# Optimization experiments

Measured on AMD Instinct MI355X. Metric: run time of the kernel, lower is better.

The kernel has to match this reference:

```python
import jax, jax.numpy as jnp
import numpy as np

B, T, V, E, H = 256, 512, 30000, 256, 32


def _run_dir(x, mask, Wih, Whh, bih, bhh, reverse):
    # x: [B,T,D], mask: [B,T] bool. PyTorch GRU gate order: r, z, n.
    gi = jnp.einsum('btd,gd->btg', x, Wih) + bih  # precompute input gates [B,T,3H]
    h0 = jnp.zeros((x.shape[0], Whh.shape[1]), x.dtype)

    def step(h, inp):
        gi_t, m_t = inp
        gh = h @ Whh.T + bhh
        ir, iz, inn = jnp.split(gi_t, 3, axis=-1)
        hr, hz, hn = jnp.split(gh, 3, axis=-1)
        r = jax.nn.sigmoid(ir + hr)
        z = jax.nn.sigmoid(iz + hz)
        n = jnp.tanh(inn + r * hn)
        h_new = (1.0 - z) * n + z * h
        # packed-sequence semantics: freeze state at padded steps
        h = jnp.where(m_t[:, None], h_new, h)
        return h, h

    hT, ys = jax.lax.scan(step, h0, (jnp.swapaxes(gi, 0, 1), mask.T), reverse=reverse)
    return jnp.swapaxes(ys, 0, 1), hT  # outputs [B,T,H], final hidden [B,H]


def _bigru_layer(x, mask, pf, pb):
    of, hf = _run_dir(x, mask, *pf, reverse=False)
    ob, hb = _run_dir(x, mask, *pb, reverse=True)
    return jnp.concatenate([of, ob], axis=-1), hf, hb


def setup_inputs() -> dict:
    key = jax.random.key(0)
    ks = jax.random.split(key, 24)
    lengths = jax.random.randint(ks[0], (B,), 1, T + 1)
    mask = (jnp.arange(T)[None, :] < lengths[:, None]).astype(jnp.int32)
    ids = jax.random.randint(ks[1], (B, T), 1, V)
    ids = jnp.where(mask > 0, ids, 0)  # pad_id = 0 at padded positions
    embed = (jax.random.normal(ks[2], (V, E), jnp.float32) * 0.1).at[0].set(0.0)

    def gru_params(k, din):
        k1, k2, k3, k4 = jax.random.split(k, 4)
        s = 1.0 / np.sqrt(H)
        return (jax.random.uniform(k1, (3 * H, din), jnp.float32, -s, s),
                jax.random.uniform(k2, (3 * H, H), jnp.float32, -s, s),
                jax.random.uniform(k3, (3 * H,), jnp.float32, -s, s),
                jax.random.uniform(k4, (3 * H,), jnp.float32, -s, s))

    inp = {"input_ids": ids, "attention_mask": mask, "embed": embed}
    i = 3
    for layer, din in (("l0", E), ("l1", 2 * H)):
        for d in ("f", "b"):
            Wih, Whh, bih, bhh = gru_params(ks[i], din); i += 1
            inp[f"Wih_{layer}{d}"] = Wih
            inp[f"Whh_{layer}{d}"] = Whh
            inp[f"bih_{layer}{d}"] = bih
            inp[f"bhh_{layer}{d}"] = bhh
    s = 1.0 / np.sqrt(2 * H)
    inp["Wout"] = jax.random.uniform(ks[i], (6, 2 * H), jnp.float32, -s, s)
    inp["bout"] = jax.random.uniform(ks[i + 1], (6,), jnp.float32, -s, s)
    return inp


def reference(input_ids, attention_mask, embed,
              Wih_l0f, Whh_l0f, bih_l0f, bhh_l0f,
              Wih_l0b, Whh_l0b, bih_l0b, bhh_l0b,
              Wih_l1f, Whh_l1f, bih_l1f, bhh_l1f,
              Wih_l1b, Whh_l1b, bih_l1b, bhh_l1b,
              Wout, bout):
    mask = attention_mask > 0
    x = embed[input_ids]  # [B,T,E]
    x1, _, _ = _bigru_layer(x, mask,
                            (Wih_l0f, Whh_l0f, bih_l0f, bhh_l0f),
                            (Wih_l0b, Whh_l0b, bih_l0b, bhh_l0b))
    # no dropout: eval-mode forward
    _, hf, hb = _bigru_layer(x1, mask,
                             (Wih_l1f, Whh_l1f, bih_l1f, bhh_l1f),
                             (Wih_l1b, Whh_l1b, bih_l1b, bhh_l1b))
    top = jnp.concatenate([hf, hb], axis=-1)  # h_n[-2:] -> [B, 2H]
    return top @ Wout.T + bout  # [B, 6]
```

## Files before the change

### kernel.cpp

```cpp
#include <hip/hip_runtime.h>
#include <hip/hip_bf16.h>
#include <stdint.h>

#define B_ 256
#define T_ 512
#define V_ 30000
#define E_ 256
#define H_ 32

typedef float v2f __attribute__((ext_vector_type(2)));

__device__ __forceinline__ float sigmoidf_fast(float x) {
    return 1.0f / (1.0f + __expf(-x));
}
__device__ __forceinline__ float tanhf_fast(float x) {
    return 1.0f - 2.0f / (1.0f + __expf(2.0f * x));
}
__device__ __forceinline__ uint32_t rlu(float v, int lane) {
    return (uint32_t)__builtin_amdgcn_readlane(__float_as_int(v), lane);
}
__device__ __forceinline__ void pk_fma(v2f& acc, v2f w, uint64_t hh) {
    asm("v_pk_fma_f32 %0, %1, %2, %0" : "+v"(acc) : "v"(w), "s"(hh));
}

#define GEMM_MT 64
#define GEMM_KC 32
#define GEMM_PA 68
#define GEMM_PB 196

__global__ __launch_bounds__(256) void gemm_gates(
    const float* __restrict__ A, int M, int K,
    const float* __restrict__ Wf, const float* __restrict__ Wb,
    const float* __restrict__ bihf, const float* __restrict__ bhhf,
    const float* __restrict__ bihb, const float* __restrict__ bhhb,
    float* __restrict__ Out)
{
    __shared__ float As[GEMM_KC][GEMM_PA];
    __shared__ float Bs[GEMM_KC][GEMM_PB];

    const int tid = threadIdx.x;
    const int mbase = blockIdx.x * GEMM_MT;
    const int mg = tid >> 5, ng = tid & 31;
    const int m_off = mg * 8, n_off = ng * 6;

    float acc[8][6];
    #pragma unroll
    for (int r = 0; r < 8; ++r)
        #pragma unroll
        for (int c = 0; c < 6; ++c) acc[r][c] = 0.f;

    for (int kc = 0; kc < K; kc += GEMM_KC) {
        #pragma unroll
        for (int i = 0; i < 2; ++i) {
            int fi = tid + 256 * i;
            int row = fi >> 3, cf = fi & 7;
            int m = mbase + row;
            float4 v = make_float4(0.f, 0.f, 0.f, 0.f);
            if (m < M) v = *(const float4*)&A[(size_t)m * K + kc + cf * 4];
            As[cf * 4 + 0][row] = v.x; As[cf * 4 + 1][row] = v.y;
            As[cf * 4 + 2][row] = v.z; As[cf * 4 + 3][row] = v.w;
        }
        #pragma unroll
        for (int i = 0; i < 6; ++i) {
            int fi = tid + 256 * i;
            int g = fi >> 3, cf = fi & 7;
            const float* Wsel = (g < 96) ? (Wf + (size_t)g * K)
                                         : (Wb + (size_t)(g - 96) * K);
            float4 v = *(const float4*)&Wsel[kc + cf * 4];
            Bs[cf * 4 + 0][g] = v.x; Bs[cf * 4 + 1][g] = v.y;
            Bs[cf * 4 + 2][g] = v.z; Bs[cf * 4 + 3][g] = v.w;
        }
        __syncthreads();
        #pragma unroll
        for (int k = 0; k < GEMM_KC; ++k) {
            float a[8], bb[6];
            *(float4*)&a[0] = *(const float4*)&As[k][m_off];
            *(float4*)&a[4] = *(const float4*)&As[k][m_off + 4];
            *(float2*)&bb[0] = *(const float2*)&Bs[k][n_off];
            *(float2*)&bb[2] = *(const float2*)&Bs[k][n_off + 2];
            *(float2*)&bb[4] = *(const float2*)&Bs[k][n_off + 4];
            #pragma unroll
            for (int r = 0; r < 8; ++r)
                #pragma unroll
                for (int c = 0; c < 6; ++c)
                    acc[r][c] = fmaf(a[r], bb[c], acc[r][c]);
        }
        __syncthreads();
    }

    float bias[6];
    #pragma unroll
    for (int c = 0; c < 6; ++c) {
        int g = n_off + c;
        int g96 = (g < 96) ? g : g - 96;
        const float* bih = (g < 96) ? bihf : bihb;
        const float* bhh = (g < 96) ? bhhf : bhhb;
        bias[c] = bih[g96] + ((g96 < 64) ? bhh[g96] : 0.f);
    }
    #pragma unroll
    for (int r = 0; r < 8; ++r) {
        int m = mbase + m_off + r;
        if (m < M) {
            float* op = &Out[(size_t)m * 192 + n_off];
            #pragma unroll
            for (int c = 0; c < 6; ++c) op[c] = acc[r][c] + bias[c];
        }
    }
}

template <int USE_IDS>
__global__ __launch_bounds__(64, 1) void gru_scan(
    const float* __restrict__ gi,
    const int* __restrict__ ids,
    const int* __restrict__ mask,
    const float* __restrict__ Whh_f, const float* __restrict__ Whh_b,
    const float* __restrict__ bhh_f, const float* __restrict__ bhh_b,
    float* __restrict__ out_seq,
    float* __restrict__ out_fin)
{
    const int l = threadIdx.x;
    const int j = l & 31;
    const bool lower = l < 32;
    const int dir = blockIdx.x & 1;
    const int b = blockIdx.x >> 1;
    const int bT = b * T_;

    const float* Whh = dir ? Whh_b : Whh_f;
    const float* bhh = dir ? bhh_b : bhh_f;

    v2f wR[16], wZ[16], wN[16];
    #pragma unroll
    for (int q = 0; q < 16; ++q) {
        wR[q] = *(const v2f*)&Whh[j * 32 + 2 * q];
        wZ[q] = *(const v2f*)&Whh[(32 + j) * 32 + 2 * q];
        wN[q] = *(const v2f*)&Whh[(64 + j) * 32 + 2 * q];
    }
    const float bn = bhh[64 + j];

    const int offR = dir * 96 + j;
    const int offZ = dir * 96 + 32 + j;
    const int offN = dir * 96 + 64 + j;

    auto wbase = [&](int c) { return dir ? (bT + 508 - 4 * c) : (bT + 4 * c); };

    int4 ids0 = make_int4(0, 0, 0, 0);
    if (USE_IDS) ids0 = *(const int4*)&ids[wbase(0)];
    int4 mask_use = *(const int4*)&mask[wbase(0)];
    int4 mask_mid = *(const int4*)&mask[wbase(1)];
    int4 mask_in  = make_int4(0, 0, 0, 0);
    int4 ids_pf = make_int4(0, 0, 0, 0), ids_mid = ids_pf, ids_in = ids_pf;
    if (USE_IDS) {
        ids_pf  = *(const int4*)&ids[wbase(1)];
        ids_mid = *(const int4*)&ids[wbase(2)];
    }

    float gR[2][4], gZ[2][4], gN[2][4];
    #pragma unroll
    for (int u = 0; u < 4; ++u) {
        int row;
        if (USE_IDS) {
            const int* ip = (const int*)&ids0;
            row = dir ? ip[3 - u] : ip[u];
        } else {
            row = bT + (dir ? (511 - u) : u);
        }
        const float* gp = gi + (size_t)row * 192;
        gR[0][u] = gp[offR];
        gZ[0][u] = gp[offZ];
        gN[0][u] = gp[offN];
    }

    float h = 0.f;

    for (int c2 = 0; c2 < 64; ++c2) {
        #pragma unroll
        for (int p = 0; p < 2; ++p) {
            const int c = 2 * c2 + p;
            if (USE_IDS) {
                const int ci = (c + 3 < 128) ? (c + 3) : 127;
                ids_in = *(const int4*)&ids[wbase(ci)];
            }
            {
                const int cm = (c + 2 < 128) ? (c + 2) : 127;
                mask_in = *(const int4*)&mask[wbase(cm)];
            }
            const int cN = (c + 1 < 128) ? (c + 1) : 127;

            #pragma unroll
            for (int u = 0; u < 4; ++u) {
                int rowN;
                if (USE_IDS) {
                    const int* ip = (const int*)&ids_pf;
                    rowN = dir ? ip[3 - u] : ip[u];
                } else {
                    rowN = bT + (dir ? (511 - 4 * cN - u) : (4 * cN + u));
                }
                const float* gpN = gi + (size_t)rowN * 192;
                gR[p ^ 1][u] = gpN[offR];
                gZ[p ^ 1][u] = gpN[offZ];
                gN[p ^ 1][u] = gpN[offN];

                const int* mu = (const int*)&mask_use;
                const int m = dir ? mu[3 - u] : mu[u];

                v2f aR = {0.f, 0.f}, aZ = {0.f, 0.f}, aN = {0.f, 0.f};
                #pragma unroll
                for (int k = 0; k < 16; ++k) {
                    const uint32_t hlo = rlu(h, 2 * k);
                    const uint32_t hhi = rlu(h, 2 * k + 1);
                    const uint64_t hh = ((uint64_t)hhi << 32) | hlo;
                    pk_fma(aR, wR[k], hh);
                    pk_fma(aZ, wZ[k], hh);
                    pk_fma(aN, wN[k], hh);
                }
                const float r  = sigmoidf_fast(gR[p][u] + aR.x + aR.y);
                const float z  = sigmoidf_fast(gZ[p][u] + aZ.x + aZ.y);
                const float hn = bn + aN.x + aN.y;
                const float n  = tanhf_fast(gN[p][u] + r * hn);
                const float hnew = n + z * (h - n);
                h = m ? hnew : h;

                if (out_seq != nullptr) {
                    const int t = dir ? (511 - 4 * c - u) : (4 * c + u);
                    if (lower)
                        out_seq[(size_t)(bT + t) * 64 + dir * 32 + j] = h;
                }
            }
            mask_use = mask_mid; mask_mid = mask_in;
            if (USE_IDS) { ids_pf = ids_mid; ids_mid = ids_in; }
        }
    }

    if (out_fin != nullptr && lower)
        out_fin[b * 64 + dir * 32 + j] = h;
}

__global__ void head_kernel(const float* __restrict__ hfin,
                            const float* __restrict__ Wout,
                            const float* __restrict__ bout,
                            float* __restrict__ out)
{
    int idx = blockIdx.x * blockDim.x + threadIdx.x;
    if (idx >= B_ * 6) return;
    int b = idx / 6, o = idx % 6;
    float acc = bout[o];
    const float* hp = hfin + b * 64;
    const float* wp = Wout + o * 64;
    #pragma unroll
    for (int k = 0; k < 64; ++k) acc = fmaf(hp[k], wp[k], acc);
    out[idx] = acc;
}

extern "C" void kernel_launch(void* const* d_in, const int* in_sizes, int n_in,
                              void* d_out, int out_size, void* d_ws, size_t ws_size,
                              hipStream_t stream)
{
    const int*   ids   = (const int*)d_in[0];
    const int*   mask  = (const int*)d_in[1];
    const float* embed = (const float*)d_in[2];
    const float* Wih0f = (const float*)d_in[3];
    const float* Whh0f = (const float*)d_in[4];
    const float* bih0f = (const float*)d_in[5];
    const float* bhh0f = (const float*)d_in[6];
    const float* Wih0b = (const float*)d_in[7];
    const float* Whh0b = (const float*)d_in[8];
    const float* bih0b = (const float*)d_in[9];
    const float* bhh0b = (const float*)d_in[10];
    const float* Wih1f = (const float*)d_in[11];
    const float* Whh1f = (const float*)d_in[12];
    const float* bih1f = (const float*)d_in[13];
    const float* bhh1f = (const float*)d_in[14];
    const float* Wih1b = (const float*)d_in[15];
    const float* Whh1b = (const float*)d_in[16];
    const float* bih1b = (const float*)d_in[17];
    const float* bhh1b = (const float*)d_in[18];
    const float* Wout  = (const float*)d_in[19];
    const float* bout  = (const float*)d_in[20];

    float* ws   = (float*)d_ws;
    float* gbuf = ws;
    float* x1   = ws + (size_t)B_ * T_ * 192;
    float* hfin = x1 + (size_t)B_ * T_ * 64;

    gemm_gates<<<(V_ + GEMM_MT - 1) / GEMM_MT, 256, 0, stream>>>(
        embed, V_, E_, Wih0f, Wih0b, bih0f, bhh0f, bih0b, bhh0b, gbuf);

    gru_scan<1><<<2 * B_, 64, 0, stream>>>(
        gbuf, ids, mask, Whh0f, Whh0b, bhh0f, bhh0b, x1, nullptr);

    gemm_gates<<<(B_ * T_) / GEMM_MT, 256, 0, stream>>>(
        x1, B_ * T_, 64, Wih1f, Wih1b, bih1f, bhh1f, bih1b, bhh1b, gbuf);

    gru_scan<0><<<2 * B_, 64, 0, stream>>>(
        gbuf, nullptr, mask, Whh1f, Whh1b, bhh1f, bhh1b, nullptr, hfin);

    head_kernel<<<(B_ * 6 + 255) / 256, 256, 0, stream>>>(hfin, Wout, bout,
                                                          (float*)d_out);
}
```

Before: 563.4 us.

## Pack two sequences per wave in GRU scan and share hidden state through LDS

Each 64-lane block of the GRU scan now handles two batch elements, one per half-wave, instead of duplicating one sequence across both halves. This halves the grid. The hidden-state broadcast for the recurrent matvec changes from 32 scalar readlanes per step to an LDS write followed by vector float4 reads. The aim is to stop wasting the upper half-wave and to shorten the serial dependency chain per step. In exchange, every timestep now pays an LDS round-trip latency, and only half as many waves are available to hide latency.

```diff
diff --git a/kernel.cpp b/kernel.cpp
--- a/kernel.cpp
+++ b/kernel.cpp
@@ -16,11 +16,8 @@
 __device__ __forceinline__ float tanhf_fast(float x) {
     return 1.0f - 2.0f / (1.0f + __expf(2.0f * x));
 }
-__device__ __forceinline__ uint32_t rlu(float v, int lane) {
-    return (uint32_t)__builtin_amdgcn_readlane(__float_as_int(v), lane);
-}
-__device__ __forceinline__ void pk_fma(v2f& acc, v2f w, uint64_t hh) {
-    asm("v_pk_fma_f32 %0, %1, %2, %0" : "+v"(acc) : "v"(w), "s"(hh));
+__device__ __forceinline__ void pk_fma(v2f& acc, v2f w, v2f h) {
+    asm("v_pk_fma_f32 %0, %1, %2, %0" : "+v"(acc) : "v"(w), "v"(h));
 }
 
 #define GEMM_MT 64
@@ -118,11 +115,13 @@
     float* __restrict__ out_seq,
     float* __restrict__ out_fin)
 {
+    __shared__ float hsh[64];
+
     const int l = threadIdx.x;
     const int j = l & 31;
-    const bool lower = l < 32;
+    const int half = l >> 5;
     const int dir = blockIdx.x & 1;
-    const int b = blockIdx.x >> 1;
+    const int b = (blockIdx.x >> 1) * 2 + half;
     const int bT = b * T_;
 
     const float* Whh = dir ? Whh_b : Whh_f;
@@ -203,15 +202,22 @@
                 const int* mu = (const int*)&mask_use;
                 const int m = dir ? mu[3 - u] : mu[u];
 
+                hsh[l] = h;
+                const float* hb = &hsh[half * 32];
+                v2f hr[16];
+                #pragma unroll
+                for (int q = 0; q < 8; ++q) {
+                    float4 hv = *(const float4*)&hb[4 * q];
+                    hr[2 * q]     = (v2f){hv.x, hv.y};
+                    hr[2 * q + 1] = (v2f){hv.z, hv.w};
+                }
+
                 v2f aR = {0.f, 0.f}, aZ = {0.f, 0.f}, aN = {0.f, 0.f};
                 #pragma unroll
                 for (int k = 0; k < 16; ++k) {
-                    const uint32_t hlo = rlu(h, 2 * k);
-                    const uint32_t hhi = rlu(h, 2 * k + 1);
-                    const uint64_t hh = ((uint64_t)hhi << 32) | hlo;
-                    pk_fma(aR, wR[k], hh);
-                    pk_fma(aZ, wZ[k], hh);
-                    pk_fma(aN, wN[k], hh);
+                    pk_fma(aR, wR[k], hr[k]);
+                    pk_fma(aZ, wZ[k], hr[k]);
+                    pk_fma(aN, wN[k], hr[k]);
                 }
                 const float r  = sigmoidf_fast(gR[p][u] + aR.x + aR.y);
                 const float z  = sigmoidf_fast(gZ[p][u] + aZ.x + aZ.y);
@@ -222,8 +228,7 @@
 
                 if (out_seq != nullptr) {
                     const int t = dir ? (511 - 4 * c - u) : (4 * c + u);
-                    if (lower)
-                        out_seq[(size_t)(bT + t) * 64 + dir * 32 + j] = h;
+                    out_seq[(size_t)(bT + t) * 64 + dir * 32 + j] = h;
                 }
             }
             mask_use = mask_mid; mask_mid = mask_in;
@@ -231,7 +236,7 @@
         }
     }
 
-    if (out_fin != nullptr && lower)
+    if (out_fin != nullptr)
         out_fin[b * 64 + dir * 32 + j] = h;
 }
 
@@ -285,13 +290,13 @@
     gemm_gates<<<(V_ + GEMM_MT - 1) / GEMM_MT, 256, 0, stream>>>(
         embed, V_, E_, Wih0f, Wih0b, bih0f, bhh0f, bih0b, bhh0b, gbuf);
 
-    gru_scan<1><<<2 * B_, 64, 0, stream>>>(
+    gru_scan<1><<<B_, 64, 0, stream>>>(
         gbuf, ids, mask, Whh0f, Whh0b, bhh0f, bhh0b, x1, nullptr);
 
     gemm_gates<<<(B_ * T_) / GEMM_MT, 256, 0, stream>>>(
         x1, B_ * T_, 64, Wih1f, Wih1b, bih1f, bhh1f, bih1b, bhh1b, gbuf);
 
-    gru_scan<0><<<2 * B_, 64, 0, stream>>>(
+    gru_scan<0><<<B_, 64, 0, stream>>>(
         gbuf, nullptr, mask, Whh1f, Whh1b, bhh1f, bhh1b, nullptr, hfin);
 
     head_kernel<<<(B_ * 6 + 255) / 256, 256, 0, stream>>>(hfin, Wout, bout,
```

Result: faster. 529.9 us (-5.9%).

## Replace readlane hidden-state broadcast with DPP swizzles and LDS exchange

Applied to the files above, without the earlier changes.

The recurrent matvec no longer broadcasts each hidden element through 32 serial readlanes into SGPRs. Each lane now gathers its own 16-lane group's values with DPP row mirrors/swizzles, using permuted weight columns to match, and reads the other 16 values from a small LDS buffer written every step. The log2(e) and 2·log2(e) scales are folded into the recurrent weights and the input-gate GEMM output, so the gate nonlinearities map straight onto raw v_exp_f32/v_rcp_f32. This targets the serial per-step latency of the scan. In exchange it relies on in-wave LDS ordering without a barrier and on more register-held weights.

```diff
diff --git a/kernel.cpp b/kernel.cpp
--- a/kernel.cpp
+++ b/kernel.cpp
@@ -10,18 +10,27 @@
 
 typedef float v2f __attribute__((ext_vector_type(2)));
 
-__device__ __forceinline__ float sigmoidf_fast(float x) {
-    return 1.0f / (1.0f + __expf(-x));
-}
-__device__ __forceinline__ float tanhf_fast(float x) {
-    return 1.0f - 2.0f / (1.0f + __expf(2.0f * x));
-}
-__device__ __forceinline__ uint32_t rlu(float v, int lane) {
-    return (uint32_t)__builtin_amdgcn_readlane(__float_as_int(v), lane);
-}
-__device__ __forceinline__ void pk_fma(v2f& acc, v2f w, uint64_t hh) {
-    asm("v_pk_fma_f32 %0, %1, %2, %0" : "+v"(acc) : "v"(w), "s"(hh));
-}
+#define LOG2E_F 1.44269504088896340736f
+
+__device__ __forceinline__ float exp2_fast(float x) {
+    float r; asm("v_exp_f32 %0, %1" : "=v"(r) : "v"(x)); return r;
+}
+__device__ __forceinline__ float rcp_fast(float x) {
+    float r; asm("v_rcp_f32 %0, %1" : "=v"(r) : "v"(x)); return r;
+}
+__device__ __forceinline__ void pk_fma(v2f& acc, v2f w, v2f h) {
+    asm("v_pk_fma_f32 %0, %1, %2, %0" : "+v"(acc) : "v"(w), "v"(h));
+}
+template <int CTRL>
+__device__ __forceinline__ float mdpp(float x) {
+    return __int_as_float(
+        __builtin_amdgcn_mov_dpp(__float_as_int(x), CTRL, 0xF, 0xF, true));
+}
+#define DPP_XOR1  0xB1
+#define DPP_XOR2  0x4E
+#define DPP_XOR3  0x1B
+#define DPP_XOR7  0x141
+#define DPP_XOR15 0x140
 
 #define GEMM_MT 64
 #define GEMM_KC 32
@@ -88,7 +97,7 @@
         __syncthreads();
     }
 
-    float bias[6];
+    float bias[6], gsc[6];
     #pragma unroll
     for (int c = 0; c < 6; ++c) {
         int g = n_off + c;
@@ -96,6 +105,7 @@
         const float* bih = (g < 96) ? bihf : bihb;
         const float* bhh = (g < 96) ? bhhf : bhhb;
         bias[c] = bih[g96] + ((g96 < 64) ? bhh[g96] : 0.f);
+        gsc[c]  = (g96 < 64) ? -LOG2E_F : 2.0f * LOG2E_F;
     }
     #pragma unroll
     for (int r = 0; r < 8; ++r) {
@@ -103,7 +113,7 @@
         if (m < M) {
             float* op = &Out[(size_t)m * 192 + n_off];
             #pragma unroll
-            for (int c = 0; c < 6; ++c) op[c] = acc[r][c] + bias[c];
+            for (int c = 0; c < 6; ++c) op[c] = (acc[r][c] + bias[c]) * gsc[c];
         }
     }
 }
@@ -118,7 +128,11 @@
     float* __restrict__ out_seq,
     float* __restrict__ out_fin)
 {
+    __shared__ float hsh[64];
+
     const int l = threadIdx.x;
+    const int i16 = l & 15;
+    const int rp = (l >> 4) & 1;
     const int j = l & 31;
     const bool lower = l < 32;
     const int dir = blockIdx.x & 1;
@@ -128,14 +142,33 @@
     const float* Whh = dir ? Whh_b : Whh_f;
     const float* bhh = dir ? bhh_b : bhh_f;
 
-    v2f wR[16], wZ[16], wN[16];
-    #pragma unroll
-    for (int q = 0; q < 16; ++q) {
-        wR[q] = *(const v2f*)&Whh[j * 32 + 2 * q];
-        wZ[q] = *(const v2f*)&Whh[(32 + j) * 32 + 2 * q];
-        wN[q] = *(const v2f*)&Whh[(64 + j) * 32 + 2 * q];
-    }
-    const float bn = bhh[64 + j];
+    const int kA = 16 * rp;
+    const int kB = 16 - kA;
+
+    const float sRZ = -LOG2E_F;
+    const float sN2 = 2.0f * LOG2E_F;
+
+    const int M0[8] = {0, 2, 7, 5, 15, 13, 8, 10};
+    const int M1[8] = {1, 3, 6, 4, 14, 12, 9, 11};
+
+    v2f wAR[8], wAZ[8], wAN[8], wBR[8], wBZ[8], wBN[8];
+    #pragma unroll
+    for (int q = 0; q < 8; ++q) {
+        const int ka0 = kA + (i16 ^ M0[q]);
+        const int ka1 = kA + (i16 ^ M1[q]);
+        wAR[q] = (v2f){Whh[j * 32 + ka0] * sRZ, Whh[j * 32 + ka1] * sRZ};
+        wAZ[q] = (v2f){Whh[(32 + j) * 32 + ka0] * sRZ,
+                       Whh[(32 + j) * 32 + ka1] * sRZ};
+        wAN[q] = (v2f){Whh[(64 + j) * 32 + ka0] * sN2,
+                       Whh[(64 + j) * 32 + ka1] * sN2};
+        v2f br = *(const v2f*)&Whh[j * 32 + kB + 2 * q];
+        v2f bz = *(const v2f*)&Whh[(32 + j) * 32 + kB + 2 * q];
+        v2f bn_ = *(const v2f*)&Whh[(64 + j) * 32 + kB + 2 * q];
+        wBR[q] = (v2f){br.x * sRZ, br.y * sRZ};
+        wBZ[q] = (v2f){bz.x * sRZ, bz.y * sRZ};
+        wBN[q] = (v2f){bn_.x * sN2, bn_.y * sN2};
+    }
+    const float bns = bhh[64 + j] * sN2;
 
     const int offR = dir * 96 + j;
     const int offZ = dir * 96 + 32 + j;
@@ -171,11 +204,12 @@
     }
 
     float h = 0.f;
+    hsh[l] = 0.f;
 
     for (int c2 = 0; c2 < 64; ++c2) {
         #pragma unroll
-        for (int p = 0; p < 2; ++p) {
-            const int c = 2 * c2 + p;
+        for (int pb = 0; pb < 2; ++pb) {
+            const int c = 2 * c2 + pb;
             if (USE_IDS) {
                 const int ci = (c + 3 < 128) ? (c + 3) : 127;
                 ids_in = *(const int4*)&ids[wbase(ci)];
@@ -196,29 +230,71 @@
                     rowN = bT + (dir ? (511 - 4 * cN - u) : (4 * cN + u));
                 }
                 const float* gpN = gi + (size_t)rowN * 192;
-                gR[p ^ 1][u] = gpN[offR];
-                gZ[p ^ 1][u] = gpN[offZ];
-                gN[p ^ 1][u] = gpN[offN];
+                gR[pb ^ 1][u] = gpN[offR];
+                gZ[pb ^ 1][u] = gpN[offZ];
+                gN[pb ^ 1][u] = gpN[offN];
 
                 const int* mu = (const int*)&mask_use;
                 const int m = dir ? mu[3 - u] : mu[u];
 
-                v2f aR = {0.f, 0.f}, aZ = {0.f, 0.f}, aN = {0.f, 0.f};
+                float4 o0 = *(const float4*)&hsh[kB + 0];
+                float4 o1 = *(const float4*)&hsh[kB + 4];
+                float4 o2 = *(const float4*)&hsh[kB + 8];
+                float4 o3 = *(const float4*)&hsh[kB + 12];
+
+                v2f p[8];
+                p[0].x = h;                      p[0].y = mdpp<DPP_XOR1>(h);
+                p[1].x = mdpp<DPP_XOR2>(h);      p[1].y = mdpp<DPP_XOR3>(h);
+                p[2].x = mdpp<DPP_XOR7>(h);      p[2].y = mdpp<DPP_XOR7>(p[0].y);
+                p[3].x = mdpp<DPP_XOR7>(p[1].x); p[3].y = mdpp<DPP_XOR7>(p[1].y);
+                p[4].x = mdpp<DPP_XOR15>(h);     p[4].y = mdpp<DPP_XOR15>(p[0].y);
+                p[5].x = mdpp<DPP_XOR15>(p[1].x); p[5].y = mdpp<DPP_XOR15>(p[1].y);
+                p[6].x = mdpp<DPP_XOR15>(p[2].x); p[6].y = mdpp<DPP_XOR15>(p[2].y);
+                p[7].x = mdpp<DPP_XOR15>(p[3].x); p[7].y = mdpp<DPP_XOR15>(p[3].y);
+
+                v2f aAR = {0.f, 0.f}, aAZ = {0.f, 0.f}, aAN = {0.f, 0.f};
                 #pragma unroll
-                for (int k = 0; k < 16; ++k) {
-                    const uint32_t hlo = rlu(h, 2 * k);
-                    const uint32_t hhi = rlu(h, 2 * k + 1);
-                    const uint64_t hh = ((uint64_t)hhi << 32) | hlo;
-                    pk_fma(aR, wR[k], hh);
-                    pk_fma(aZ, wZ[k], hh);
-                    pk_fma(aN, wN[k], hh);
-                }
-                const float r  = sigmoidf_fast(gR[p][u] + aR.x + aR.y);
-                const float z  = sigmoidf_fast(gZ[p][u] + aZ.x + aZ.y);
-                const float hn = bn + aN.x + aN.y;
-                const float n  = tanhf_fast(gN[p][u] + r * hn);
+                for (int q = 0; q < 8; ++q) {
+                    pk_fma(aAR, wAR[q], p[q]);
+                    pk_fma(aAZ, wAZ[q], p[q]);
+                    pk_fma(aAN, wAN[q], p[q]);
+                }
+
+                v2f hB[8];
+                hB[0] = (v2f){o0.x, o0.y}; hB[1] = (v2f){o0.z, o0.w};
+                hB[2] = (v2f){o1.x, o1.y}; hB[3] = (v2f){o1.z, o1.w};
+                hB[4] = (v2f){o2.x, o2.y}; hB[5] = (v2f){o2.z, o2.w};
+                hB[6] = (v2f){o3.x, o3.y}; hB[7] = (v2f){o3.z, o3.w};
+
+                v2f aB0R = {0.f, 0.f}, aB0Z = {0.f, 0.f}, aB0N = {0.f, 0.f};
+                v2f aB1R = {0.f, 0.f}, aB1Z = {0.f, 0.f}, aB1N = {0.f, 0.f};
+                #pragma unroll
+                for (int q = 0; q < 4; ++q) {
+                    pk_fma(aB0R, wBR[q], hB[q]);
+                    pk_fma(aB0Z, wBZ[q], hB[q]);
+                    pk_fma(aB0N, wBN[q], hB[q]);
+                }
+                #pragma unroll
+                for (int q = 4; q < 8; ++q) {
+                    pk_fma(aB1R, wBR[q], hB[q]);
+                    pk_fma(aB1Z, wBZ[q], hB[q]);
+                    pk_fma(aB1N, wBN[q], hB[q]);
+                }
+
+                const float yr = (gR[pb][u] + (aAR.x + aAR.y)) +
+                                 ((aB0R.x + aB0R.y) + (aB1R.x + aB1R.y));
+                const float yz = (gZ[pb][u] + (aAZ.x + aAZ.y)) +
+                                 ((aB0Z.x + aB0Z.y) + (aB1Z.x + aB1Z.y));
+                const float hns = (bns + (aAN.x + aAN.y)) +
+                                  ((aB0N.x + aB0N.y) + (aB1N.x + aB1N.y));
+                const float r = rcp_fast(1.0f + exp2_fast(yr));
+                const float z = rcp_fast(1.0f + exp2_fast(yz));
+                const float yn = gN[pb][u] + r * hns;
+                const float n = fmaf(-2.0f, rcp_fast(1.0f + exp2_fast(yn)), 1.0f);
                 const float hnew = n + z * (h - n);
                 h = m ? hnew : h;
+
+                hsh[l] = h;
 
                 if (out_seq != nullptr) {
                     const int t = dir ? (511 - 4 * c - u) : (4 * c + u);
```

New measurement: 528.4 us. 6.2% less time.
